# Kernel tuning notes

Measured on AMD Instinct MI355X. Metric: run time of the kernel, lower is better.

## Reference

```python
import jax, jax.numpy as jnp
import numpy as np

N = 50000
E = 1600000


def gcn_conv(x, W, b, src, dst, edge_weight):
    # PyG GCNConv(normalize=False): h = x @ W.T; msg_e = h[src_e] * w_e;
    # out_i = sum_{e: dst_e = i} msg_e + bias
    h = x @ W.T                                   # [N, C_out]
    msg = h[src]                                  # [E, C_out]
    if edge_weight is not None:
        msg = msg * edge_weight[:, None]
    agg = jax.ops.segment_sum(msg, dst, num_segments=N)  # [N, C_out]
    return agg + b


def batchnorm_eval(x, gamma, beta, mean, var, eps=1e-5):
    inv = gamma * jax.lax.rsqrt(var + eps)
    return (x - mean) * inv + beta


def setup_inputs() -> dict:
    key = jax.random.key(0)
    ks = jax.random.split(key, 16)
    d = {}
    d["x"] = jax.random.normal(ks[0], (N, 128), dtype=jnp.float32)
    d["edge_index"] = jax.random.randint(ks[1], (2, E), 0, N, dtype=jnp.int64)
    d["edge_attr"] = jax.random.uniform(ks[2], (E, 8), dtype=jnp.float32)
    # layer 1: 128 -> 256, layer 2: 256 -> 256, layer 3: 256 -> 256
    s1 = 1.0 / np.sqrt(128.0)
    s2 = 1.0 / np.sqrt(256.0)
    d["W1"] = jax.random.uniform(ks[3], (256, 128), jnp.float32, -s1, s1)
    d["b1"] = jnp.zeros((256,), jnp.float32)
    d["g1"] = jnp.ones((256,), jnp.float32)
    d["beta1"] = jnp.zeros((256,), jnp.float32)
    d["m1"] = jax.random.normal(ks[4], (256,), jnp.float32) * 0.1
    d["v1"] = jax.random.uniform(ks[5], (256,), jnp.float32, minval=0.5, maxval=1.5)
    d["W2"] = jax.random.uniform(ks[6], (256, 256), jnp.float32, -s2, s2)
    d["b2"] = jnp.zeros((256,), jnp.float32)
    d["g2"] = jnp.ones((256,), jnp.float32)
    d["beta2"] = jnp.zeros((256,), jnp.float32)
    d["m2"] = jax.random.normal(ks[7], (256,), jnp.float32) * 0.1
    d["v2"] = jax.random.uniform(ks[8], (256,), jnp.float32, minval=0.5, maxval=1.5)
    d["W3"] = jax.random.uniform(ks[9], (256, 256), jnp.float32, -s2, s2)
    d["b3"] = jnp.zeros((256,), jnp.float32)
    return d


def reference(x, edge_index, edge_attr, W1, b1, g1, beta1, m1, v1,
              W2, b2, g2, beta2, m2, v2, W3, b3):
    src, dst = edge_index[0], edge_index[1]
    ew = jnp.mean(edge_attr, axis=-1)            # [E], torch.mean(edge_attr, dim=-1)
    h = gcn_conv(x, W1, b1, src, dst, ew)
    h = jax.nn.relu(batchnorm_eval(h, g1, beta1, m1, v1))
    h = gcn_conv(h, W2, b2, src, dst, ew)
    h = jax.nn.relu(batchnorm_eval(h, g2, beta2, m2, v2))
    out = gcn_conv(h, W3, b3, src, dst, None)    # last layer: no edge_weight
    return out
```

## Files before the change

### kernel.cpp

```cpp
#include <hip/hip_runtime.h>
#include <cstdint>
#include <cstddef>

#define NN 50000
#define EE 1600000
#define KB ((NN + 127) / 128)
#define PCHUNK 4096
#define SLICE 8064
#define GPAD 32
#define GBLK 2048

typedef __attribute__((ext_vector_type(8))) short short8;
typedef __attribute__((ext_vector_type(8))) unsigned short ushort8;
typedef __attribute__((ext_vector_type(4))) float float4v;
typedef __attribute__((ext_vector_type(2))) float floatx2;

__device__ __forceinline__ float bf2f(unsigned short u) {
    union { unsigned int i; float f; } v; v.i = ((unsigned int)u) << 16; return v.f;
}
__device__ __forceinline__ unsigned short f2bf(float f) {
    union { float f; unsigned int i; } v; v.f = f;
    unsigned int r = v.i + 0x7FFF + ((v.i >> 16) & 1);
    return (unsigned short)(r >> 16);
}

__global__ __launch_bounds__(256) void cvt_all_kernel(
    const float* __restrict__ x, unsigned short* __restrict__ xb,
    const float* __restrict__ w1, unsigned short* __restrict__ o1,
    const float* __restrict__ w2, unsigned short* __restrict__ o2,
    const float* __restrict__ w3, unsigned short* __restrict__ o3,
    int* __restrict__ gbcnt)
{
    const int blk = blockIdx.x;
    if (blk < 6250) {
        int i = (blk * 256 + threadIdx.x) * 4;
        float4 v = *(const float4*)(x + i);
        ushort4 o;
        o.x = f2bf(v.x); o.y = f2bf(v.y); o.z = f2bf(v.z); o.w = f2bf(v.w);
        *(ushort4*)(xb + i) = o;
    } else if (blk < 6410) {
        int i = ((blk - 6250) * 256 + threadIdx.x) * 4;
        const float* in; unsigned short* out;
        if (i < 32768) { in = w1; out = o1; }
        else if (i < 32768 + 65536) { in = w2; out = o2; i -= 32768; }
        else { in = w3; out = o3; i -= 32768 + 65536; }
        float4 v = *(const float4*)(in + i);
        ushort4 o;
        o.x = f2bf(v.x); o.y = f2bf(v.y); o.z = f2bf(v.z); o.w = f2bf(v.w);
        *(ushort4*)(out + i) = o;
    } else {
        int i = (blk - 6410) * 256 + threadIdx.x;
        if (i < KB * GPAD) gbcnt[i] = 0;
    }
}

__global__ __launch_bounds__(256) void passA_kernel(
    const int* __restrict__ src, const int* __restrict__ dst,
    const float* __restrict__ ea, int* __restrict__ gbcnt,
    uint2* __restrict__ tmp, int E)
{
    __shared__ int bh[KB];
    __shared__ int bbase[KB];
    const int t = threadIdx.x;
    const int base_e = blockIdx.x * PCHUNK;
    for (int i = t; i < KB; i += 256) bh[i] = 0;
    __syncthreads();

    unsigned int rlo[16]; int dd[16];
    #pragma unroll
    for (int u = 0; u < 16; u++) {
        int e = base_e + u * 256 + t;
        dd[u] = -1;
        if (e < E) {
            int d = dst[e], s = src[e];
            if ((unsigned)d < NN && (unsigned)s < NN) {
                const float4* p = (const float4*)(ea + (size_t)e * 8);
                float4 a = p[0], b = p[1];
                float w = (a.x + a.y + a.z + a.w + b.x + b.y + b.z + b.w) * 0.125f;
                rlo[u] = (unsigned)s | ((unsigned)f2bf(w) << 16);
                dd[u] = d;
                atomicAdd(&bh[d >> 7], 1);
            }
        }
    }
    __syncthreads();
    for (int i = t; i < KB; i += 256) {
        int c = bh[i];
        bbase[i] = (c > 0) ? atomicAdd(&gbcnt[i * GPAD], c) : 0;
        bh[i] = 0;
    }
    __syncthreads();
    #pragma unroll
    for (int u = 0; u < 16; u++) {
        if (dd[u] >= 0) {
            int b = dd[u] >> 7;
            int pos = bbase[b] + atomicAdd(&bh[b], 1);
            if (pos < SLICE)
                tmp[(size_t)b * SLICE + pos] = (uint2){rlo[u], (unsigned)(dd[u] & 127)};
        }
    }
}

__global__ __launch_bounds__(256) void passB_kernel(
    const uint2* __restrict__ tmp, const int* __restrict__ gbcnt,
    int* __restrict__ rowptr, unsigned int* __restrict__ recs)
{
    __shared__ int cnts[KB];
    __shared__ int lh[128];
    __shared__ int lp[128];
    __shared__ int sboff;
    const int b = blockIdx.x;
    const int t = threadIdx.x;
    for (int i = t; i < KB; i += 256) cnts[i] = gbcnt[i * GPAD];
    if (t < 128) lh[t] = 0;
    __syncthreads();
    if (t == 0) {
        int s = 0;
        for (int i = 0; i < b; i++) s += cnts[i];
        sboff = s;
        if (b == KB - 1) rowptr[NN] = s + cnts[b];
    }
    __syncthreads();
    int cnt = cnts[b]; if (cnt > SLICE) cnt = SLICE;
    const uint2* slice = tmp + (size_t)b * SLICE;
    for (int i = t; i < cnt; i += 256) atomicAdd(&lh[slice[i].y], 1);
    __syncthreads();
    if (t < 128) lp[t] = lh[t];
    __syncthreads();
    #pragma unroll
    for (int off = 1; off < 128; off <<= 1) {
        int v = 0;
        if (t < 128 && t >= off) v = lp[t - off];
        __syncthreads();
        if (t < 128) lp[t] += v;
        __syncthreads();
    }
    const int node0 = b * 128;
    const int nnodes = (NN - node0 < 128) ? (NN - node0) : 128;
    if (t < nnodes) {
        int excl = lp[t] - lh[t] + sboff;
        rowptr[node0 + t] = excl;
        lh[t] = excl;
    }
    __syncthreads();
    for (int i = t; i < cnt; i += 256) {
        uint2 r = slice[i];
        int pos = atomicAdd(&lh[r.y], 1);
        recs[pos] = r.x;
    }
}

template <bool HASW>
__global__ __launch_bounds__(256) void gather_bf(
    const unsigned short* __restrict__ h, const int* __restrict__ rowptr,
    const unsigned int* __restrict__ recs, unsigned short* __restrict__ agg)
{
    const int wave = threadIdx.x >> 6;
    const int lane = threadIdx.x & 63;
    const int quar = lane >> 4;
    const int l16  = lane & 15;

    for (int node = blockIdx.x * 4 + wave; node < NN; node += GBLK * 4) {
        int beg = rowptr[node], end = rowptr[node + 1];
        float a[8] = {0.f, 0.f, 0.f, 0.f, 0.f, 0.f, 0.f, 0.f};
        int j = beg;
        for (; j + 16 <= end; j += 16) {
            unsigned int r[4]; ushort8 v[4];
            #pragma unroll
            for (int u = 0; u < 4; u++) r[u] = recs[j + 4 * u + quar];
            #pragma unroll
            for (int u = 0; u < 4; u++)
                v[u] = *(const ushort8*)(h + (size_t)(r[u] & 0xFFFF) * 128 + l16 * 8);
            #pragma unroll
            for (int u = 0; u < 4; u++) {
                float w = HASW ? bf2f((unsigned short)(r[u] >> 16)) : 1.f;
                #pragma unroll
                for (int k = 0; k < 8; k++) a[k] += w * bf2f(v[u][k]);
            }
        }
        for (; j < end; j += 4) {
            int idx = j + quar;
            unsigned int r = recs[idx < end ? idx : end - 1];
            float w = (idx < end) ? (HASW ? bf2f((unsigned short)(r >> 16)) : 1.f) : 0.f;
            ushort8 v = *(const ushort8*)(h + (size_t)(r & 0xFFFF) * 128 + l16 * 8);
            #pragma unroll
            for (int k = 0; k < 8; k++) a[k] += w * bf2f(v[k]);
        }
        #pragma unroll
        for (int k = 0; k < 8; k++) {
            a[k] += __shfl_xor(a[k], 16, 64);
            a[k] += __shfl_xor(a[k], 32, 64);
        }
        if (quar == 0) {
            ushort8 o;
            #pragma unroll
            for (int k = 0; k < 8; k++) o[k] = f2bf(a[k]);
            *(ushort8*)(agg + (size_t)node * 128 + l16 * 8) = o;
        }
    }
}

template <bool HASW>
__global__ __launch_bounds__(256) void gather_fp8(
    const unsigned char* __restrict__ h, const int* __restrict__ rowptr,
    const unsigned int* __restrict__ recs, unsigned short* __restrict__ agg)
{
    const int wave = threadIdx.x >> 6;
    const int lane = threadIdx.x & 63;
    const int slot = lane >> 4;
    const int l16  = lane & 15;

    for (int node = blockIdx.x * 4 + wave; node < NN; node += GBLK * 4) {
        int beg = rowptr[node], end = rowptr[node + 1];
        float a[16];
        #pragma unroll
        for (int k = 0; k < 16; k++) a[k] = 0.f;
        int j = beg;
        for (; j + 16 <= end; j += 16) {
            unsigned int r[4]; uint4 v[4];
            #pragma unroll
            for (int u = 0; u < 4; u++) r[u] = recs[j + 4 * u + slot];
            #pragma unroll
            for (int u = 0; u < 4; u++)
                v[u] = *(const uint4*)(h + (size_t)(r[u] & 0xFFFF) * 256 + l16 * 16);
            #pragma unroll
            for (int u = 0; u < 4; u++) {
                float w = HASW ? bf2f((unsigned short)(r[u] >> 16)) : 1.f;
                unsigned int ww[4] = {v[u].x, v[u].y, v[u].z, v[u].w};
                #pragma unroll
                for (int wi = 0; wi < 4; wi++) {
                    floatx2 lo = __builtin_amdgcn_cvt_pk_f32_fp8(ww[wi], false);
                    floatx2 hi = __builtin_amdgcn_cvt_pk_f32_fp8(ww[wi], true);
                    a[4 * wi + 0] += w * lo.x;
                    a[4 * wi + 1] += w * lo.y;
                    a[4 * wi + 2] += w * hi.x;
                    a[4 * wi + 3] += w * hi.y;
                }
            }
        }
        for (; j < end; j += 4) {
            int idx = j + slot;
            unsigned int r = recs[idx < end ? idx : end - 1];
            float w = (idx < end) ? (HASW ? bf2f((unsigned short)(r >> 16)) : 1.f) : 0.f;
            uint4 v = *(const uint4*)(h + (size_t)(r & 0xFFFF) * 256 + l16 * 16);
            unsigned int ww[4] = {v.x, v.y, v.z, v.w};
            #pragma unroll
            for (int wi = 0; wi < 4; wi++) {
                floatx2 lo = __builtin_amdgcn_cvt_pk_f32_fp8(ww[wi], false);
                floatx2 hi = __builtin_amdgcn_cvt_pk_f32_fp8(ww[wi], true);
                a[4 * wi + 0] += w * lo.x;
                a[4 * wi + 1] += w * lo.y;
                a[4 * wi + 2] += w * hi.x;
                a[4 * wi + 3] += w * hi.y;
            }
        }
        #pragma unroll
        for (int k = 0; k < 16; k++) {
            a[k] += __shfl_xor(a[k], 16, 64);
            a[k] += __shfl_xor(a[k], 32, 64);
        }
        if (slot == 0) {
            ushort8 o0, o1;
            #pragma unroll
            for (int k = 0; k < 8; k++) { o0[k] = f2bf(a[k]); o1[k] = f2bf(a[k + 8]); }
            *(ushort8*)(agg + (size_t)node * 256 + l16 * 16) = o0;
            *(ushort8*)(agg + (size_t)node * 256 + l16 * 16 + 8) = o1;
        }
    }
}

template <int CIN, int MODE>
__global__ __launch_bounds__(256) void mm_mfma(
    const unsigned short* __restrict__ A, const unsigned short* __restrict__ W,
    const float* __restrict__ bias,
    const float* __restrict__ gamma, const float* __restrict__ beta,
    const float* __restrict__ mean, const float* __restrict__ var,
    void* __restrict__ out, int M)
{
    const int lane = threadIdx.x & 63;
    const int wave = threadIdx.x >> 6;
    const int quad = lane >> 4;
    const int l16  = lane & 15;
    const int row0 = blockIdx.x * 64;
    const int col0 = wave * 64;

    float4v acc[4][4] = {};

    for (int k0 = 0; k0 < CIN; k0 += 32) {
        const int ka = k0 + quad * 8;
        short8 af[4], bf[4];
        #pragma unroll
        for (int i = 0; i < 4; i++) {
            int r = row0 + i * 16 + l16;
            af[i] = (r < M) ? *(const short8*)(A + (size_t)r * CIN + ka) : (short8)0;
            bf[i] = *(const short8*)(W + (size_t)(col0 + i * 16 + l16) * CIN + ka);
        }
        #pragma unroll
        for (int mi = 0; mi < 4; mi++)
            #pragma unroll
            for (int ni = 0; ni < 4; ni++)
                acc[mi][ni] = __builtin_amdgcn_mfma_f32_16x16x32_bf16(
                    af[mi], bf[ni], acc[mi][ni], 0, 0, 0);
    }

    float cb[4], cmu[4], cinv[4], cbe[4];
    #pragma unroll
    for (int ni = 0; ni < 4; ni++) {
        int gc = col0 + ni * 16 + l16;
        cb[ni] = bias[gc];
        if (MODE == 1) {
            cmu[ni]  = mean[gc];
            cinv[ni] = gamma[gc] * rsqrtf(var[gc] + 1e-5f);
            cbe[ni]  = beta[gc];
        }
    }
    #pragma unroll
    for (int mi = 0; mi < 4; mi++) {
        #pragma unroll
        for (int reg = 0; reg < 4; reg++) {
            int gr = row0 + mi * 16 + quad * 4 + reg;
            if (gr >= M) continue;
            #pragma unroll
            for (int ni = 0; ni < 4; ni++) {
                int gc = col0 + ni * 16 + l16;
                float v = acc[mi][ni][reg] + cb[ni];
                if (MODE == 1) {
                    v = (v - cmu[ni]) * cinv[ni] + cbe[ni];
                    v = fmaxf(v, 0.f);
                    int pk = __builtin_amdgcn_cvt_pk_fp8_f32(v, v, 0, false);
                    ((unsigned char*)out)[(size_t)gr * 256 + gc] = (unsigned char)(pk & 0xFF);
                } else {
                    ((float*)out)[(size_t)gr * 256 + gc] = v;
                }
            }
        }
    }
}

extern "C" void kernel_launch(void* const* d_in, const int* in_sizes, int n_in,
                              void* d_out, int out_size, void* d_ws, size_t ws_size,
                              hipStream_t stream) {
    const float* x   = (const float*)d_in[0];
    const int*   ei  = (const int*)d_in[1];
    const float* ea  = (const float*)d_in[2];
    const float* W1  = (const float*)d_in[3];
    const float* b1  = (const float*)d_in[4];
    const float* g1  = (const float*)d_in[5];
    const float* be1 = (const float*)d_in[6];
    const float* m1  = (const float*)d_in[7];
    const float* v1  = (const float*)d_in[8];
    const float* W2  = (const float*)d_in[9];
    const float* b2  = (const float*)d_in[10];
    const float* g2  = (const float*)d_in[11];
    const float* be2 = (const float*)d_in[12];
    const float* m2  = (const float*)d_in[13];
    const float* v2  = (const float*)d_in[14];
    const float* W3  = (const float*)d_in[15];
    const float* b3  = (const float*)d_in[16];

    const int* src = ei;
    const int* dst = ei + EE;

    char* p = (char*)d_ws;
    auto alloc = [&](size_t bytes) { char* r = p; p += (bytes + 255) & ~255ULL; return r; };
    int*            rowptr    = (int*)alloc((NN + 1) * 4);
    int*            gbcnt     = (int*)alloc((size_t)KB * GPAD * 4);
    unsigned int*   recs      = (unsigned int*)alloc((size_t)EE * 4);
    unsigned short* xb        = (unsigned short*)alloc((size_t)NN * 128 * 2);
    unsigned short* W1b       = (unsigned short*)alloc(256 * 128 * 2);
    unsigned short* W2b       = (unsigned short*)alloc(256 * 256 * 2);
    unsigned short* W3b       = (unsigned short*)alloc(256 * 256 * 2);
    unsigned short* agg       = (unsigned short*)alloc((size_t)NN * 256 * 2);
    unsigned char*  hbuf      = (unsigned char*)alloc((size_t)NN * 256);
    float*          out       = (float*)d_out;

    uint2* tmp = (uint2*)agg;

    const int mtiles  = (NN + 63) / 64;
    const int pblocks = (EE + PCHUNK - 1) / PCHUNK;

    cvt_all_kernel<<<6459, 256, 0, stream>>>(x, xb, W1, W1b, W2, W2b, W3, W3b, gbcnt);

    passA_kernel<<<pblocks, 256, 0, stream>>>(src, dst, ea, gbcnt, tmp, EE);
    passB_kernel<<<KB, 256, 0, stream>>>(tmp, gbcnt, rowptr, recs);

    gather_bf<true><<<GBLK, 256, 0, stream>>>(xb, rowptr, recs, agg);
    mm_mfma<128, 1><<<mtiles, 256, 0, stream>>>(
        agg, W1b, b1, g1, be1, m1, v1, hbuf, NN);

    gather_fp8<true><<<GBLK, 256, 0, stream>>>(hbuf, rowptr, recs, agg);
    mm_mfma<256, 1><<<mtiles, 256, 0, stream>>>(
        agg, W2b, b2, g2, be2, m2, v2, hbuf, NN);

    gather_fp8<false><<<GBLK, 256, 0, stream>>>(hbuf, rowptr, recs, agg);
    mm_mfma<256, 0><<<mtiles, 256, 0, stream>>>(
        agg, W3b, b3, nullptr, nullptr, nullptr, nullptr, out, NN);
}
```

Baseline: 456.3 us.

## Quantize input features to fp8 and fuse conversion with edge bucketing pass

The input feature matrix is now converted to fp8 instead of bf16, and the first-layer gather reads 16 fp8 values per lane with 8 edge slots per wave, which halves gather traffic for layer 1. The conversion kernel is merged into the edge bucketing kernel via block-index dispatch, and counter zeroing moves to a memset, saving one launch. The cost is lower precision for the raw inputs, a wider shuffle reduction, and a fixed tail loop that masks out-of-range edges.

```diff
diff --git a/kernel.cpp b/kernel.cpp
--- a/kernel.cpp
+++ b/kernel.cpp
@@ -24,45 +24,42 @@
     return (unsigned short)(r >> 16);
 }
 
-__global__ __launch_bounds__(256) void cvt_all_kernel(
-    const float* __restrict__ x, unsigned short* __restrict__ xb,
+__global__ __launch_bounds__(256) void setupA_kernel(
+    const int* __restrict__ src, const int* __restrict__ dst,
+    const float* __restrict__ ea, int* __restrict__ gbcnt,
+    uint2* __restrict__ tmp,
+    const float* __restrict__ x, unsigned char* __restrict__ xb8,
     const float* __restrict__ w1, unsigned short* __restrict__ o1,
     const float* __restrict__ w2, unsigned short* __restrict__ o2,
-    const float* __restrict__ w3, unsigned short* __restrict__ o3,
-    int* __restrict__ gbcnt)
-{
-    const int blk = blockIdx.x;
-    if (blk < 6250) {
-        int i = (blk * 256 + threadIdx.x) * 4;
-        float4 v = *(const float4*)(x + i);
-        ushort4 o;
-        o.x = f2bf(v.x); o.y = f2bf(v.y); o.z = f2bf(v.z); o.w = f2bf(v.w);
-        *(ushort4*)(xb + i) = o;
-    } else if (blk < 6410) {
-        int i = ((blk - 6250) * 256 + threadIdx.x) * 4;
-        const float* in; unsigned short* out;
-        if (i < 32768) { in = w1; out = o1; }
-        else if (i < 32768 + 65536) { in = w2; out = o2; i -= 32768; }
-        else { in = w3; out = o3; i -= 32768 + 65536; }
-        float4 v = *(const float4*)(in + i);
-        ushort4 o;
-        o.x = f2bf(v.x); o.y = f2bf(v.y); o.z = f2bf(v.z); o.w = f2bf(v.w);
-        *(ushort4*)(out + i) = o;
-    } else {
-        int i = (blk - 6410) * 256 + threadIdx.x;
-        if (i < KB * GPAD) gbcnt[i] = 0;
-    }
-}
-
-__global__ __launch_bounds__(256) void passA_kernel(
-    const int* __restrict__ src, const int* __restrict__ dst,
-    const float* __restrict__ ea, int* __restrict__ gbcnt,
-    uint2* __restrict__ tmp, int E)
+    const float* __restrict__ w3, unsigned short* __restrict__ o3)
 {
     __shared__ int bh[KB];
     __shared__ int bbase[KB];
+    const int blk = blockIdx.x;
     const int t = threadIdx.x;
-    const int base_e = blockIdx.x * PCHUNK;
+
+    if (blk >= 391) {
+        if (blk < 6641) {
+            int i = ((blk - 391) * 256 + t) * 4;
+            float4 v = *(const float4*)(x + i);
+            int pk = __builtin_amdgcn_cvt_pk_fp8_f32(v.x, v.y, 0, false);
+            pk = __builtin_amdgcn_cvt_pk_fp8_f32(v.z, v.w, pk, true);
+            *(unsigned int*)(xb8 + i) = (unsigned int)pk;
+        } else {
+            int i = ((blk - 6641) * 256 + t) * 4;
+            const float* in; unsigned short* out;
+            if (i < 32768) { in = w1; out = o1; }
+            else if (i < 32768 + 65536) { in = w2; out = o2; i -= 32768; }
+            else { in = w3; out = o3; i -= 32768 + 65536; }
+            float4 v = *(const float4*)(in + i);
+            ushort4 o;
+            o.x = f2bf(v.x); o.y = f2bf(v.y); o.z = f2bf(v.z); o.w = f2bf(v.w);
+            *(ushort4*)(out + i) = o;
+        }
+        return;
+    }
+
+    const int base_e = blk * PCHUNK;
     for (int i = t; i < KB; i += 256) bh[i] = 0;
     __syncthreads();
 
@@ -71,7 +68,7 @@
     for (int u = 0; u < 16; u++) {
         int e = base_e + u * 256 + t;
         dd[u] = -1;
-        if (e < E) {
+        if (e < EE) {
             int d = dst[e], s = src[e];
             if ((unsigned)d < NN && (unsigned)s < NN) {
                 const float4* p = (const float4*)(ea + (size_t)e * 8);
@@ -150,52 +147,59 @@
     }
 }
 
-template <bool HASW>
-__global__ __launch_bounds__(256) void gather_bf(
-    const unsigned short* __restrict__ h, const int* __restrict__ rowptr,
+__global__ __launch_bounds__(256) void gather_xf8(
+    const unsigned char* __restrict__ h, const int* __restrict__ rowptr,
     const unsigned int* __restrict__ recs, unsigned short* __restrict__ agg)
 {
     const int wave = threadIdx.x >> 6;
     const int lane = threadIdx.x & 63;
-    const int quar = lane >> 4;
-    const int l16  = lane & 15;
+    const int slot = lane >> 3;
+    const int l8   = lane & 7;
 
     for (int node = blockIdx.x * 4 + wave; node < NN; node += GBLK * 4) {
         int beg = rowptr[node], end = rowptr[node + 1];
-        float a[8] = {0.f, 0.f, 0.f, 0.f, 0.f, 0.f, 0.f, 0.f};
-        int j = beg;
-        for (; j + 16 <= end; j += 16) {
-            unsigned int r[4]; ushort8 v[4];
-            #pragma unroll
-            for (int u = 0; u < 4; u++) r[u] = recs[j + 4 * u + quar];
+        float a[16];
+        #pragma unroll
+        for (int k = 0; k < 16; k++) a[k] = 0.f;
+        for (int j = beg; j < end; j += 32) {
+            unsigned int r[4]; uint4 v[4];
+            #pragma unroll
+            for (int u = 0; u < 4; u++) {
+                int idx = j + 8 * u + slot;
+                r[u] = recs[idx < end ? idx : end - 1];
+            }
             #pragma unroll
             for (int u = 0; u < 4; u++)
-                v[u] = *(const ushort8*)(h + (size_t)(r[u] & 0xFFFF) * 128 + l16 * 8);
+                v[u] = *(const uint4*)(h + (size_t)(r[u] & 0xFFFF) * 128 + l8 * 16);
             #pragma unroll
             for (int u = 0; u < 4; u++) {
-                float w = HASW ? bf2f((unsigned short)(r[u] >> 16)) : 1.f;
+                int idx = j + 8 * u + slot;
+                float w = (idx < end) ? bf2f((unsigned short)(r[u] >> 16)) : 0.f;
+                unsigned int ww[4] = {v[u].x, v[u].y, v[u].z, v[u].w};
                 #pragma unroll
-                for (int k = 0; k < 8; k++) a[k] += w * bf2f(v[u][k]);
-            }
-        }
-        for (; j < end; j += 4) {
-            int idx = j + quar;
-            unsigned int r = recs[idx < end ? idx : end - 1];
-            float w = (idx < end) ? (HASW ? bf2f((unsigned short)(r >> 16)) : 1.f) : 0.f;
-            ushort8 v = *(const ushort8*)(h + (size_t)(r & 0xFFFF) * 128 + l16 * 8);
-            #pragma unroll
-            for (int k = 0; k < 8; k++) a[k] += w * bf2f(v[k]);
-        }
-        #pragma unroll
-        for (int k = 0; k < 8; k++) {
+                for (int wi = 0; wi < 4; wi++) {
+                    floatx2 lo = __builtin_amdgcn_cvt_pk_f32_fp8(ww[wi], false);
+                    floatx2 hi = __builtin_amdgcn_cvt_pk_f32_fp8(ww[wi], true);
+                    a[4 * wi + 0] += w * lo.x;
+                    a[4 * wi + 1] += w * lo.y;
+                    a[4 * wi + 2] += w * hi.x;
+                    a[4 * wi + 3] += w * hi.y;
+                }
+            }
+        }
+        #pragma unroll
+        for (int k = 0; k < 16; k++) {
+            a[k] += __shfl_xor(a[k], 8, 64);
             a[k] += __shfl_xor(a[k], 16, 64);
             a[k] += __shfl_xor(a[k], 32, 64);
         }
-        if (quar == 0) {
-            ushort8 o;
-            #pragma unroll
-            for (int k = 0; k < 8; k++) o[k] = f2bf(a[k]);
-            *(ushort8*)(agg + (size_t)node * 128 + l16 * 8) = o;
+        if (slot == 0) {
+            ushort8 o0, o1;
+            #pragma unroll
+            for (int k = 0; k < 8; k++) { o0[k] = f2bf(a[k]); o1[k] = f2bf(a[k + 8]); }
+            unsigned short* d0 = agg + (size_t)node * 128 + l8 * 16;
+            *(ushort8*)(d0) = o0;
+            *(ushort8*)(d0 + 8) = o1;
         }
     }
 }
@@ -366,7 +370,7 @@
     int*            rowptr    = (int*)alloc((NN + 1) * 4);
     int*            gbcnt     = (int*)alloc((size_t)KB * GPAD * 4);
     unsigned int*   recs      = (unsigned int*)alloc((size_t)EE * 4);
-    unsigned short* xb        = (unsigned short*)alloc((size_t)NN * 128 * 2);
+    unsigned char*  xb8       = (unsigned char*)alloc((size_t)NN * 128);
     unsigned short* W1b       = (unsigned short*)alloc(256 * 128 * 2);
     unsigned short* W2b       = (unsigned short*)alloc(256 * 256 * 2);
     unsigned short* W3b       = (unsigned short*)alloc(256 * 256 * 2);
@@ -376,15 +380,14 @@
 
     uint2* tmp = (uint2*)agg;
 
-    const int mtiles  = (NN + 63) / 64;
-    const int pblocks = (EE + PCHUNK - 1) / PCHUNK;
-
-    cvt_all_kernel<<<6459, 256, 0, stream>>>(x, xb, W1, W1b, W2, W2b, W3, W3b, gbcnt);
-
-    passA_kernel<<<pblocks, 256, 0, stream>>>(src, dst, ea, gbcnt, tmp, EE);
+    const int mtiles = (NN + 63) / 64;
+
+    hipMemsetAsync(gbcnt, 0, (size_t)KB * GPAD * 4, stream);
+    setupA_kernel<<<6801, 256, 0, stream>>>(
+        src, dst, ea, gbcnt, tmp, x, xb8, W1, W1b, W2, W2b, W3, W3b);
     passB_kernel<<<KB, 256, 0, stream>>>(tmp, gbcnt, rowptr, recs);
 
-    gather_bf<true><<<GBLK, 256, 0, stream>>>(xb, rowptr, recs, agg);
+    gather_xf8<<<GBLK, 256, 0, stream>>>(xb8, rowptr, recs, agg);
     mm_mfma<128, 1><<<mtiles, 256, 0, stream>>>(
         agg, W1b, b1, g1, be1, m1, v1, hbuf, NN);
 
```

Result: faster. 444.5 us (-2.6%).
